# Kernel optimization log

Hardware: AMD Instinct MI355X
Metric: run time of the kernel (lower is better)

Reference implementation:

```python
import jax, jax.numpy as jnp
import numpy as np

LATENT = 1024
HIDDEN = 4096
ENC = 1024
HEADS = 16
HEAD_DIM = LATENT // HEADS
B, SQ, SK = 4, 1024, 1024
EPS = 1e-5


def _linear(x, w, b):
    # torch nn.Linear: y = x @ w.T + b, w shape (out, in)
    return jnp.einsum('bsi,oi->bso', x, w) + b


def _mha(Q, K, wq, bq, wk, bk, wv, bv, wo, bo):
    Bq, Sq, _ = Q.shape
    Sk = K.shape[1]
    Qp = _linear(Q, wq, bq).reshape(Bq, Sq, HEADS, HEAD_DIM)
    Kp = _linear(K, wk, bk).reshape(Bq, Sk, HEADS, HEAD_DIM)
    Vp = _linear(K, wv, bv).reshape(Bq, Sk, HEADS, HEAD_DIM)
    # NOTE: original scales by 1/sqrt(latent_size), not 1/sqrt(head_dim)
    E = jnp.einsum('bqhd,bkhd->bhqk', Qp, Kp) / np.sqrt(LATENT).astype(np.float32)
    A = jax.nn.softmax(E, axis=-1)
    O = jnp.einsum('bhqk,bkhd->bqhd', A, Vp).reshape(Bq, Sq, LATENT)
    return _linear(O, wo, bo)


def _ln(x, g, b):
    mu = jnp.mean(x, axis=-1, keepdims=True)
    var = jnp.mean((x - mu) ** 2, axis=-1, keepdims=True)
    return (x - mu) * jax.lax.rsqrt(var + EPS) * g + b


def setup_inputs() -> dict:
    key = jax.random.key(0)
    ks = jax.random.split(key, 32)
    s = 0.02
    d = {
        'Q': jax.random.normal(ks[0], (B, SQ, LATENT), jnp.float32),
        'K': jax.random.normal(ks[1], (B, SK, ENC), jnp.float32),
        'a1_wq': jax.random.normal(ks[2], (LATENT, LATENT)) * s,
        'a1_bq': jnp.zeros((LATENT,)),
        'a1_wk': jax.random.normal(ks[3], (LATENT, LATENT)) * s,
        'a1_bk': jnp.zeros((LATENT,)),
        'a1_wv': jax.random.normal(ks[4], (LATENT, LATENT)) * s,
        'a1_bv': jnp.zeros((LATENT,)),
        'a1_wo': jax.random.normal(ks[5], (LATENT, LATENT)) * s,
        'a1_bo': jnp.zeros((LATENT,)),
        'a2_wq': jax.random.normal(ks[6], (LATENT, LATENT)) * s,
        'a2_bq': jnp.zeros((LATENT,)),
        'a2_wk': jax.random.normal(ks[7], (LATENT, ENC)) * s,
        'a2_bk': jnp.zeros((LATENT,)),
        'a2_wv': jax.random.normal(ks[8], (LATENT, ENC)) * s,
        'a2_bv': jnp.zeros((LATENT,)),
        'a2_wo': jax.random.normal(ks[9], (LATENT, LATENT)) * s,
        'a2_bo': jnp.zeros((LATENT,)),
        'fc_w1': jax.random.normal(ks[10], (HIDDEN, LATENT)) * s,
        'fc_b1': jnp.zeros((HIDDEN,)),
        'fc_w2': jax.random.normal(ks[11], (LATENT, HIDDEN)) * s,
        'fc_b2': jnp.zeros((LATENT,)),
        'ln0_g': jnp.ones((LATENT,)), 'ln0_b': jnp.zeros((LATENT,)),
        'ln1_g': jnp.ones((LATENT,)), 'ln1_b': jnp.zeros((LATENT,)),
        'ln2_g': jnp.ones((LATENT,)), 'ln2_b': jnp.zeros((LATENT,)),
    }
    return d


def reference(Q, K, a1_wq, a1_bq, a1_wk, a1_bk, a1_wv, a1_bv, a1_wo, a1_bo,
              a2_wq, a2_bq, a2_wk, a2_bk, a2_wv, a2_bv, a2_wo, a2_bo,
              fc_w1, fc_b1, fc_w2, fc_b2,
              ln0_g, ln0_b, ln1_g, ln1_b, ln2_g, ln2_b):
    # self-attention block
    A1 = _mha(Q, Q, a1_wq, a1_bq, a1_wk, a1_bk, a1_wv, a1_bv, a1_wo, a1_bo)
    X = _ln(Q + A1, ln0_g, ln0_b)
    # cross-attention block
    A2 = _mha(X, K, a2_wq, a2_bq, a2_wk, a2_bk, a2_wv, a2_bv, a2_wo, a2_bo)
    X = _ln(X + A2, ln1_g, ln1_b)
    # FFN: Linear -> ReLU -> Linear
    FC = _linear(jax.nn.relu(_linear(X, fc_w1, fc_b1)), fc_w2, fc_b2)
    X = _ln(X + FC, ln2_g, ln2_b)
    return X
```

## Files before the change

### kernel.cpp

```cpp
#include <hip/hip_runtime.h>
#include <hip/hip_bf16.h>
#include <math.h>

#define LATENT 1024
#define HIDDEN 4096
#define HEADS 16
#define HEAD_DIM 64
#define BATCH 4
#define SQL 1024
#define SKL 1024

typedef __bf16 bf16;
typedef __attribute__((ext_vector_type(4))) __bf16 bf16x4;
typedef __attribute__((ext_vector_type(8))) __bf16 bf16x8;
typedef __attribute__((ext_vector_type(4))) float f32x4;

#define MFMA16 __builtin_amdgcn_mfma_f32_16x16x32_bf16

__device__ __forceinline__ void async_ld16(const bf16* g, bf16* l) {
    __builtin_amdgcn_global_load_lds(
        (const __attribute__((address_space(1))) unsigned int*)g,
        (__attribute__((address_space(3))) unsigned int*)l,
        16, 0, 0);
}

__global__ void detect_dtype(const void* g, int* flag) {
    if (threadIdx.x == 0) *flag = (*(const float*)g == 1.0f) ? 1 : 0;
}

struct CanonArgs {
    const void* src[28];
    bf16* dst[28];
    int n[28];
};

__global__ __launch_bounds__(256) void canonicalize(CanonArgs a, const int* flagp) {
    const int buf = blockIdx.y;
    const int n = a.n[buf];
    const int i0 = (blockIdx.x * 256 + threadIdx.x) * 8;
    if (i0 >= n) return;
    bf16* dst = a.dst[buf];
    if (*flagp) {
        const float* s = (const float*)a.src[buf];
        float4 u0 = *(const float4*)(s + i0);
        float4 u1 = *(const float4*)(s + i0 + 4);
        bf16x8 o;
        o[0] = (bf16)u0.x; o[1] = (bf16)u0.y; o[2] = (bf16)u0.z; o[3] = (bf16)u0.w;
        o[4] = (bf16)u1.x; o[5] = (bf16)u1.y; o[6] = (bf16)u1.z; o[7] = (bf16)u1.w;
        *(bf16x8*)(dst + i0) = o;
    } else {
        *(bf16x8*)(dst + i0) = *(const bf16x8*)((const bf16*)a.src[buf] + i0);
    }
}

template<bool RELU>
__global__ __launch_bounds__(256, 2)
void gemm8(const bf16* __restrict__ A, const bf16* __restrict__ W,
           const bf16* __restrict__ bias,
           bf16* __restrict__ out0, bf16* __restrict__ out1, bf16* __restrict__ outT,
           int M, int N, int K, int nNormal, int ostride) {
    constexpr int AE   = 128 * 32;
    constexpr int BE   = 256 * 32;
    constexpr int BUFE = AE + BE;
    __shared__ alignas(16) bf16 smem[3 * BUFE];
    const int tid  = threadIdx.x;
    const int w    = tid >> 6;
    const int lane = tid & 63;
    const int quad = lane >> 4;
    const int l16  = lane & 15;
    const int wrr  = w >> 1, wcc = w & 1;
    const int nx  = gridDim.x;
    const int nwg = nx * gridDim.y;
    int bid = blockIdx.y * nx + blockIdx.x;
    bid = (bid & 7) * (nwg >> 3) + (bid >> 3);
    const int bm = (bid / nx) * 128;
    const int bn = (bid % nx) * 256;

    f32x4 acc[4][8] = {};

    const bf16* gsrc[6]; int loff[6];
#pragma unroll
    for (int i = 0; i < 6; ++i) {
        const int s = tid + i * 256;
        if (s < 512) {
            const int r = s >> 2, cs = s & 3;
            gsrc[i] = A + (long)(bm + r) * K + ((cs ^ ((r >> 1) & 3)) << 3);
            loff[i] = s * 8;
        } else {
            const int sb = s - 512;
            const int r = sb >> 2, cs = sb & 3;
            gsrc[i] = W + (long)(bn + r) * K + ((cs ^ ((r >> 1) & 3)) << 3);
            loff[i] = AE + sb * 8;
        }
    }

    int offA[4], offB[8];
#pragma unroll
    for (int i = 0; i < 4; ++i) {
        const int r = wrr * 64 + i * 16 + l16;
        offA[i] = r * 32 + ((quad ^ ((r >> 1) & 3)) << 3);
    }
#pragma unroll
    for (int j = 0; j < 8; ++j) {
        const int r = wcc * 128 + j * 16 + l16;
        offB[j] = AE + r * 32 + ((quad ^ ((r >> 1) & 3)) << 3);
    }

#define STAGE_W(dst, tt)                                                       \
    {                                                                          \
        _Pragma("unroll")                                                      \
        for (int i_ = 0; i_ < 6; ++i_)                                         \
            async_ld16(gsrc[i_] + (tt) * 32, (dst) + loff[i_]);                \
    }

    const int NK = K >> 5;
    bf16 *p0 = smem, *p1 = smem + BUFE, *p2 = smem + 2 * BUFE;
    STAGE_W(p0, 0);
    STAGE_W(p1, 1);
    __asm__ volatile("s_waitcnt vmcnt(6)" ::: "memory");
    __builtin_amdgcn_s_barrier();
    __builtin_amdgcn_sched_barrier(0);

    for (int t = 0; t < NK; ++t) {
        if (t + 2 < NK) STAGE_W(p2, t + 2);
        bf16x8 af[4], bfv[8];
#pragma unroll
        for (int i = 0; i < 4; ++i) af[i]  = *(const bf16x8*)&p0[offA[i]];
#pragma unroll
        for (int j = 0; j < 8; ++j) bfv[j] = *(const bf16x8*)&p0[offB[j]];
#pragma unroll
        for (int j = 0; j < 8; ++j)
#pragma unroll
            for (int i = 0; i < 4; ++i)
                acc[i][j] = MFMA16(af[i], bfv[j], acc[i][j], 0, 0, 0);
        if (t + 2 < NK) {
            __asm__ volatile("s_waitcnt vmcnt(6)" ::: "memory");
        } else if (t + 1 < NK) {
            __asm__ volatile("s_waitcnt vmcnt(0)" ::: "memory");
        }
        if (t + 1 < NK) {
            __builtin_amdgcn_s_barrier();
            __builtin_amdgcn_sched_barrier(0);
        }
        bf16* tp = p0; p0 = p1; p1 = p2; p2 = tp;
    }
#undef STAGE_W

    float bvv[8];
#pragma unroll
    for (int j = 0; j < 8; ++j) bvv[j] = (float)bias[bn + wcc * 128 + j * 16 + l16];

    if (bn < nNormal) {
#pragma unroll
        for (int j = 0; j < 8; ++j) {
            const int colj = bn + wcc * 128 + j * 16;
            bf16* basej = out0;
            int cb = colj;
            if (out1 && cb >= 1024) { basej = out1; cb -= 1024; }
#pragma unroll
            for (int i = 0; i < 4; ++i) {
#pragma unroll
                for (int r = 0; r < 4; ++r) {
                    const int row = bm + wrr * 64 + i * 16 + quad * 4 + r;
                    float v = acc[i][j][r] + bvv[j];
                    if (RELU) v = fmaxf(v, 0.f);
                    basej[(long)row * ostride + cb + l16] = (bf16)v;
                }
            }
        }
    } else {
        const int n0v = bn - nNormal;
        __syncthreads();
#pragma unroll
        for (int p = 0; p < 4; ++p) {
            if (p) __syncthreads();
            if (wcc == (p >> 1)) {
#pragma unroll
                for (int i = 0; i < 4; ++i)
#pragma unroll
                    for (int jl = 0; jl < 4; ++jl) {
                        const int j = (p & 1) * 4 + jl;
                        const int colL = jl * 16 + l16;
                        const int rowL = wrr * 64 + i * 16 + quad * 4;
                        bf16x4 pk;
#pragma unroll
                        for (int r = 0; r < 4; ++r) pk[r] = (bf16)(acc[i][j][r] + bvv[j]);
                        *(bf16x4*)&smem[colL * 136 + rowL] = pk;
                    }
            }
            __syncthreads();
#pragma unroll
            for (int k = 0; k < 8; ++k) {
                const int c = tid + k * 256;
                const int rT = c >> 5, ch = c & 31;
                *(bf16x4*)&outT[(long)(n0v + p * 64 + rT) * M + bm + ch * 4] =
                    *(const bf16x4*)&smem[rT * 136 + ch * 4];
            }
        }
    }
}

template<int BN, bool RELU>
__global__ __launch_bounds__(256, 2)
void gemm2(const bf16* __restrict__ A, const bf16* __restrict__ W,
           const bf16* __restrict__ bias,
           bf16* __restrict__ out0, bf16* __restrict__ out1, bf16* __restrict__ outT,
           int M, int N, int K, int nNormal, int ostride) {
    constexpr int WAVES_N = BN / 64;
    constexpr int WAVES_M = 4 / WAVES_N;
    constexpr int WM = 128 / WAVES_M;
    constexpr int MI = WM / 16;
    constexpr int AE    = 128 * 64;
    constexpr int SLOTS = (128 + BN) * 8;
    constexpr int LPT   = SLOTS / 256;
    constexpr int BUFSZ = (128 + BN) * 64;
    __shared__ alignas(16) bf16 smem[2 * BUFSZ];
    const int tid  = threadIdx.x;
    const int w    = tid >> 6;
    const int lane = tid & 63;
    const int quad = lane >> 4;
    const int l16  = lane & 15;
    const int bm = blockIdx.y * 128;
    const int bn = blockIdx.x * BN;
    const int wr = w / WAVES_N, wc = w % WAVES_N;
    const int pp = l16 >> 1;

    f32x4 acc[MI][4] = {};

    const bf16* gsrc[LPT]; int loff[LPT];
#pragma unroll
    for (int i = 0; i < LPT; ++i) {
        const int s = tid + i * 256;
        if (s < 1024) {
            const int r = s >> 3, cs = s & 7;
            gsrc[i] = A + (long)(bm + r) * K + ((cs ^ ((r >> 1) & 7)) << 3);
            loff[i] = s * 8;
        } else {
            const int sb = s - 1024;
            const int r = sb >> 3, cs = sb & 7;
            gsrc[i] = W + (long)(bn + r) * K + ((cs ^ ((r >> 1) & 7)) << 3);
            loff[i] = AE + sb * 8;
        }
    }

    int offA[MI], offB[4];
#pragma unroll
    for (int i = 0; i < MI; ++i)
        offA[i] = (wr * WM + i * 16 + l16) * 64 + ((quad ^ pp) << 3);
#pragma unroll
    for (int j = 0; j < 4; ++j)
        offB[j] = AE + (wc * 64 + j * 16 + l16) * 64 + ((quad ^ pp) << 3);

#define STAGE_G(bufp, kk)                                                      \
    {                                                                          \
        bf16* bb_ = smem + (bufp) * BUFSZ;                                     \
        _Pragma("unroll")                                                      \
        for (int i_ = 0; i_ < LPT; ++i_)                                       \
            async_ld16(gsrc[i_] + (kk), bb_ + loff[i_]);                       \
    }

    STAGE_G(0, 0);
    __asm__ volatile("s_waitcnt vmcnt(0)" ::: "memory");
    __builtin_amdgcn_s_barrier();
    __builtin_amdgcn_sched_barrier(0);

    int cur = 0;
    for (int k0 = 0; k0 < K; k0 += 64) {
        if (k0 + 64 < K) STAGE_G(cur ^ 1, k0 + 64);
        const bf16* lbuf = smem + cur * BUFSZ;
#pragma unroll
        for (int ks = 0; ks < 2; ++ks) {
            bf16x8 af[MI], bfv[4];
#pragma unroll
            for (int i = 0; i < MI; ++i)
                af[i] = *(const bf16x8*)&lbuf[offA[i] ^ (ks << 5)];
#pragma unroll
            for (int j = 0; j < 4; ++j)
                bfv[j] = *(const bf16x8*)&lbuf[offB[j] ^ (ks << 5)];
#pragma unroll
            for (int i = 0; i < MI; ++i)
#pragma unroll
                for (int j = 0; j < 4; ++j)
                    acc[i][j] = MFMA16(af[i], bfv[j], acc[i][j], 0, 0, 0);
        }
        __asm__ volatile("s_waitcnt vmcnt(0)" ::: "memory");
        __builtin_amdgcn_s_barrier();
        __builtin_amdgcn_sched_barrier(0);
        cur ^= 1;
    }
#undef STAGE_G

    float bvv[4];
#pragma unroll
    for (int j = 0; j < 4; ++j) bvv[j] = (float)bias[bn + wc * 64 + j * 16 + l16];

    if (bn < nNormal) {
        bf16* base = out0;
        int colb = bn;
        if (out1 && colb >= 1024) { base = out1; colb -= 1024; }
#pragma unroll
        for (int i = 0; i < MI; ++i) {
#pragma unroll
            for (int r = 0; r < 4; ++r) {
                const int row = bm + wr * WM + i * 16 + quad * 4 + r;
#pragma unroll
                for (int j = 0; j < 4; ++j) {
                    float v = acc[i][j][r] + bvv[j];
                    if (RELU) v = fmaxf(v, 0.f);
                    base[(long)row * ostride + colb + wc * 64 + j * 16 + l16] = (bf16)v;
                }
            }
        }
    } else {
        const int n0v = bn - nNormal;
        __syncthreads();
#pragma unroll
        for (int p = 0; p < 2; ++p) {
            if (p) __syncthreads();
            if (wc == p) {
#pragma unroll
                for (int i = 0; i < MI; ++i)
#pragma unroll
                    for (int j = 0; j < 4; ++j) {
                        const int colL = j * 16 + l16;
                        const int rowL = wr * WM + i * 16 + quad * 4;
                        bf16x4 pk;
#pragma unroll
                        for (int r = 0; r < 4; ++r) pk[r] = (bf16)(acc[i][j][r] + bvv[j]);
                        *(bf16x4*)&smem[colL * 136 + rowL] = pk;
                    }
            }
            __syncthreads();
#pragma unroll
            for (int k = 0; k < 8; ++k) {
                const int c = tid + k * 256;
                const int rL = c >> 5, ch = c & 31;
                *(bf16x4*)&outT[(long)(n0v + p * 64 + rL) * M + bm + ch * 4] =
                    *(const bf16x4*)&smem[rL * 136 + ch * 4];
            }
        }
    }
}

__global__ __launch_bounds__(256, 3)
void attn2(const bf16* __restrict__ Qp, const bf16* __restrict__ Kp,
           const bf16* __restrict__ Vt, bf16* __restrict__ O) {
    __shared__ alignas(16) bf16 lQ[64 * 64];
    __shared__ alignas(16) bf16 lK[2][64 * 64];
    __shared__ alignas(16) bf16 lV[2][64 * 64];
    __shared__ alignas(16) bf16 lP[4][16 * 64];
    const int tid  = threadIdx.x;
    const int w    = tid >> 6;
    const int lane = tid & 63;
    const int quad = lane >> 4;
    const int l16  = lane & 15;
    const int pp   = l16 >> 1;
    const int b  = blockIdx.z;
    const int h  = blockIdx.y;
    const int q0 = blockIdx.x * 64;

#pragma unroll
    for (int s = 0; s < 2; ++s) {
        const int c = w * 128 + s * 64 + lane;
        const int row = c >> 3;
        const int ch = (((c & 7) ^ ((row >> 1) & 7)) << 3);
        async_ld16(Qp + (long)(b * SQL + q0 + row) * LATENT + h * 64 + ch, lQ + c * 8);
    }
#define STAGE_KV(buf, kt)                                                        \
    {                                                                            \
        _Pragma("unroll")                                                        \
        for (int s = 0; s < 2; ++s) {                                            \
            const int c = w * 128 + s * 64 + lane;                               \
            const int row = c >> 3;                                              \
            const int ch = (((c & 7) ^ ((row >> 1) & 7)) << 3);                  \
            async_ld16(Kp + (long)(b * SKL + (kt) * 64 + row) * LATENT + h * 64 + ch, \
                       &lK[buf][c * 8]);                                         \
            async_ld16(Vt + (long)(h * 64 + row) * (BATCH * SKL) + b * SKL + (kt) * 64 + ch, \
                       &lV[buf][c * 8]);                                         \
        }                                                                        \
    }
    STAGE_KV(0, 0);
    __syncthreads();

    const int aqoff = (w * 16 + l16) * 64 + ((quad ^ pp) << 3);
    bf16x8 aq[2];
    aq[0] = *(const bf16x8*)&lQ[aqoff];
    aq[1] = *(const bf16x8*)&lQ[aqoff ^ 32];
    int kvb[4];
#pragma unroll
    for (int j = 0; j < 4; ++j)
        kvb[j] = (j * 16 + l16) * 64 + ((quad ^ pp) << 3);
    const int apb = l16 * 64 + ((quad ^ pp) << 3);

    f32x4 o_acc[4] = {};
    float lsum[4] = {0.f, 0.f, 0.f, 0.f};

    for (int kt = 0; kt < SKL / 64; ++kt) {
        const int cur = kt & 1;
        if (kt < SKL / 64 - 1) STAGE_KV(cur ^ 1, kt + 1);

        f32x4 s4[4] = {};
        __builtin_amdgcn_s_setprio(1);
#pragma unroll
        for (int ks = 0; ks < 2; ++ks)
#pragma unroll
            for (int j = 0; j < 4; ++j) {
                bf16x8 bk = *(const bf16x8*)&lK[cur][kvb[j] ^ (ks << 5)];
                s4[j] = MFMA16(aq[ks], bk, s4[j], 0, 0, 0);
            }
        __builtin_amdgcn_s_setprio(0);

#pragma unroll
        for (int r = 0; r < 4; ++r) {
            const int psx = ((quad * 2 + (r >> 1)) & 7) << 3;
#pragma unroll
            for (int j = 0; j < 4; ++j) {
                const float p = __expf(s4[j][r] * 0.03125f);
                lsum[r] += p;
                lP[w][(quad * 4 + r) * 64 + ((j * 16 + l16) ^ psx)] = (bf16)p;
            }
        }
        __asm__ volatile("s_waitcnt lgkmcnt(0)" ::: "memory");

        __builtin_amdgcn_s_setprio(1);
#pragma unroll
        for (int ks = 0; ks < 2; ++ks) {
            bf16x8 ap = *(const bf16x8*)&lP[w][apb ^ (ks << 5)];
#pragma unroll
            for (int j = 0; j < 4; ++j) {
                bf16x8 bv = *(const bf16x8*)&lV[cur][kvb[j] ^ (ks << 5)];
                o_acc[j] = MFMA16(ap, bv, o_acc[j], 0, 0, 0);
            }
        }
        __builtin_amdgcn_s_setprio(0);
        __syncthreads();
    }

#pragma unroll
    for (int r = 0; r < 4; ++r) {
#pragma unroll
        for (int off = 1; off <= 8; off <<= 1)
            lsum[r] += __shfl_xor(lsum[r], off, 64);
    }
#pragma unroll
    for (int r = 0; r < 4; ++r) {
        const float inv = 1.f / lsum[r];
        const int row = q0 + w * 16 + quad * 4 + r;
#pragma unroll
        for (int j = 0; j < 4; ++j)
            O[(long)(b * SQL + row) * LATENT + h * 64 + j * 16 + l16] = (bf16)(o_acc[j][r] * inv);
    }
#undef STAGE_KV
}

template<bool F32OUT>
__global__ __launch_bounds__(256)
void ln_kernel(const bf16* __restrict__ res, const bf16* __restrict__ y,
               const bf16* __restrict__ g, const bf16* __restrict__ bta,
               bf16* __restrict__ outres, void* __restrict__ outb) {
    const int row = blockIdx.x;
    const int tid = threadIdx.x;
    const long base = (long)row * LATENT;
    const int c = tid * 4;
    bf16x4 rv = *(const bf16x4*)&res[base + c];
    bf16x4 yv = *(const bf16x4*)&y[base + c];
    float x[4];
    float s1 = 0.f, s2 = 0.f;
#pragma unroll
    for (int i = 0; i < 4; ++i) {
        float v = (float)rv[i] + (float)yv[i];
        x[i] = v; s1 += v; s2 += v * v;
    }
#pragma unroll
    for (int off = 32; off >= 1; off >>= 1) {
        s1 += __shfl_xor(s1, off, 64);
        s2 += __shfl_xor(s2, off, 64);
    }
    __shared__ float ps1[4], ps2[4];
    const int w = tid >> 6, lane = tid & 63;
    if (lane == 0) { ps1[w] = s1; ps2[w] = s2; }
    __syncthreads();
    s1 = ps1[0] + ps1[1] + ps1[2] + ps1[3];
    s2 = ps2[0] + ps2[1] + ps2[2] + ps2[3];
    const float mu = s1 * (1.f / LATENT);
    const float var = s2 * (1.f / LATENT) - mu * mu;
    const float rstd = rsqrtf(var + 1e-5f);
    bf16x4 gv = *(const bf16x4*)&g[c];
    bf16x4 bv = *(const bf16x4*)&bta[c];
    float o[4];
#pragma unroll
    for (int i = 0; i < 4; ++i)
        o[i] = (x[i] - mu) * rstd * (float)gv[i] + (float)bv[i];
    if (F32OUT) {
        float4 f; f.x = o[0]; f.y = o[1]; f.z = o[2]; f.w = o[3];
        *(float4*)&((float*)outb)[base + c] = f;
    } else {
        bf16x4 bo;
#pragma unroll
        for (int i = 0; i < 4; ++i) bo[i] = (bf16)o[i];
        *(bf16x4*)&((bf16*)outb)[base + c] = bo;
        if (outres) *(bf16x4*)&outres[base + c] = bo;
    }
}

extern "C" void kernel_launch(void* const* d_in, const int* in_sizes, int n_in,
                              void* d_out, int out_size, void* d_ws, size_t ws_size,
                              hipStream_t stream) {
    char* ws = (char*)d_ws;

    static const int order[28] = {2, 4, 6, 3, 5, 7, 12, 14, 13, 15,
                                  0, 1, 8, 9, 10, 11, 16, 17, 18, 19,
                                  20, 21, 22, 23, 24, 25, 26, 27};
    size_t coff[28];
    size_t cur = 256;
    for (int k = 0; k < 28; ++k) {
        const int i = order[k];
        coff[i] = cur;
        cur += (((size_t)in_sizes[i] * 2) + 255) & ~(size_t)255;
    }
    const size_t canon_end = (cur + 255) & ~(size_t)255;
    const size_t MB8 = 8ull << 20;
    const size_t need = canon_end + 7 * MB8;
    const bool full = ws_size >= need;

    const bf16* cv[28];
    if (full) {
        int* flag = (int*)ws;
        detect_dtype<<<dim3(1), dim3(64), 0, stream>>>(d_in[22], flag);
        CanonArgs ca;
        for (int i = 0; i < 28; ++i) {
            ca.src[i] = d_in[i];
            ca.dst[i] = (bf16*)(ws + coff[i]);
            ca.n[i]   = in_sizes[i];
            cv[i]     = (const bf16*)(ws + coff[i]);
        }
        canonicalize<<<dim3(2048, 28), dim3(256), 0, stream>>>(ca, flag);
    } else {
        for (int i = 0; i < 28; ++i) cv[i] = (const bf16*)d_in[i];
    }

    const size_t base = full ? canon_end : 0;
    bf16* Xres = (bf16*)(ws + base);
    bf16* Yf   = (bf16*)(ws + base + 1 * MB8);
    bf16* Xb   = (bf16*)(ws + base + 2 * MB8);
    bf16* Qp   = (bf16*)(ws + base + 3 * MB8);
    bf16* Kp   = (bf16*)(ws + base + 4 * MB8);
    bf16* Vt   = (bf16*)(ws + base + 5 * MB8);
    bf16* AttO = (bf16*)(ws + base + 6 * MB8);
    bf16* H    = Qp;

    const bf16 *Qc = cv[0], *Kc = cv[1];
    const int M = BATCH * SQL;
    dim3 blk(256);
    dim3 ga(SQL / 64, HEADS, BATCH);

    gemm8<false><<<dim3(3072 / 256, M / 128), blk, 0, stream>>>(
        Qc, cv[2], cv[3], Qp, Kp, Vt, M, 3072, LATENT, 2048, 1024);
    attn2<<<ga, blk, 0, stream>>>(Qp, Kp, Vt, AttO);
    gemm2<64, false><<<dim3(1024 / 64, M / 128), blk, 0, stream>>>(
        AttO, cv[8], cv[9], Yf, nullptr, nullptr, M, 1024, LATENT, 1024, 1024);
    ln_kernel<false><<<dim3(M), blk, 0, stream>>>(Qc, Yf, cv[22], cv[23], Xres, Xb);

    gemm2<64, false><<<dim3(1024 / 64, M / 128), blk, 0, stream>>>(
        Xb, cv[10], cv[11], Qp, nullptr, nullptr, M, 1024, LATENT, 1024, 1024);
    gemm8<false><<<dim3(2048 / 256, M / 128), blk, 0, stream>>>(
        Kc, cv[12], cv[13], Kp, nullptr, Vt, M, 2048, LATENT, 1024, 1024);
    attn2<<<ga, blk, 0, stream>>>(Qp, Kp, Vt, AttO);
    gemm2<64, false><<<dim3(1024 / 64, M / 128), blk, 0, stream>>>(
        AttO, cv[16], cv[17], Yf, nullptr, nullptr, M, 1024, LATENT, 1024, 1024);
    ln_kernel<false><<<dim3(M), blk, 0, stream>>>(Xres, Yf, cv[24], cv[25], Xres, Xb);

    gemm8<true><<<dim3(4096 / 256, M / 128), blk, 0, stream>>>(
        Xb, cv[18], cv[19], H, nullptr, nullptr, M, HIDDEN, LATENT, 4096, 4096);
    gemm2<64, false><<<dim3(1024 / 64, M / 128), blk, 0, stream>>>(
        H, cv[20], cv[21], Yf, nullptr, nullptr, M, 1024, HIDDEN, 1024, 1024);
    ln_kernel<true><<<dim3(M), blk, 0, stream>>>(Xres, Yf, cv[26], cv[27], nullptr, d_out);
}
```

Before: 480.7 us.

## Process 128 query rows per attention block to reuse K/V tiles

Each attention workgroup now handles 128 query rows instead of 64, with every wave computing two 16-row query tiles against the same K/V tiles held in LDS. This halves the global K/V traffic and the LDS K/V staging per query row, and gives each wave more independent MFMA work. In exchange it uses more registers and LDS (launch bounds drop to 2 blocks per CU), and the grid shrinks to 512 blocks, which lowers occupancy and parallelism.

Result: faster. 471.2 us (-2.0%).

```diff
diff --git a/kernel.cpp b/kernel.cpp
--- a/kernel.cpp
+++ b/kernel.cpp
@@ -342,13 +342,13 @@
     }
 }
 
-__global__ __launch_bounds__(256, 3)
+__global__ __launch_bounds__(256, 2)
 void attn2(const bf16* __restrict__ Qp, const bf16* __restrict__ Kp,
            const bf16* __restrict__ Vt, bf16* __restrict__ O) {
-    __shared__ alignas(16) bf16 lQ[64 * 64];
+    __shared__ alignas(16) bf16 lQ[128 * 64];
     __shared__ alignas(16) bf16 lK[2][64 * 64];
     __shared__ alignas(16) bf16 lV[2][64 * 64];
-    __shared__ alignas(16) bf16 lP[4][16 * 64];
+    __shared__ alignas(16) bf16 lP[4][32 * 64];
     const int tid  = threadIdx.x;
     const int w    = tid >> 6;
     const int lane = tid & 63;
@@ -357,11 +357,11 @@
     const int pp   = l16 >> 1;
     const int b  = blockIdx.z;
     const int h  = blockIdx.y;
-    const int q0 = blockIdx.x * 64;
-
-#pragma unroll
-    for (int s = 0; s < 2; ++s) {
-        const int c = w * 128 + s * 64 + lane;
+    const int q0 = blockIdx.x * 128;
+
+#pragma unroll
+    for (int s = 0; s < 4; ++s) {
+        const int c = s * 256 + tid;
         const int row = c >> 3;
         const int ch = (((c & 7) ^ ((row >> 1) & 7)) << 3);
         async_ld16(Qp + (long)(b * SQL + q0 + row) * LATENT + h * 64 + ch, lQ + c * 8);
@@ -382,42 +382,54 @@
     STAGE_KV(0, 0);
     __syncthreads();
 
-    const int aqoff = (w * 16 + l16) * 64 + ((quad ^ pp) << 3);
-    bf16x8 aq[2];
-    aq[0] = *(const bf16x8*)&lQ[aqoff];
-    aq[1] = *(const bf16x8*)&lQ[aqoff ^ 32];
+    bf16x8 aq0[2], aq1[2];
+    {
+        const int b0 = (w * 32 + l16) * 64 + ((quad ^ pp) << 3);
+        aq0[0] = *(const bf16x8*)&lQ[b0];
+        aq0[1] = *(const bf16x8*)&lQ[b0 ^ 32];
+        const int b1 = (w * 32 + 16 + l16) * 64 + ((quad ^ pp) << 3);
+        aq1[0] = *(const bf16x8*)&lQ[b1];
+        aq1[1] = *(const bf16x8*)&lQ[b1 ^ 32];
+    }
     int kvb[4];
 #pragma unroll
     for (int j = 0; j < 4; ++j)
         kvb[j] = (j * 16 + l16) * 64 + ((quad ^ pp) << 3);
     const int apb = l16 * 64 + ((quad ^ pp) << 3);
 
-    f32x4 o_acc[4] = {};
-    float lsum[4] = {0.f, 0.f, 0.f, 0.f};
+    f32x4 o_acc0[4] = {}, o_acc1[4] = {};
+    float lsum0[4] = {0.f, 0.f, 0.f, 0.f};
+    float lsum1[4] = {0.f, 0.f, 0.f, 0.f};
 
     for (int kt = 0; kt < SKL / 64; ++kt) {
         const int cur = kt & 1;
         if (kt < SKL / 64 - 1) STAGE_KV(cur ^ 1, kt + 1);
 
-        f32x4 s4[4] = {};
+        f32x4 s40[4] = {}, s41[4] = {};
         __builtin_amdgcn_s_setprio(1);
 #pragma unroll
         for (int ks = 0; ks < 2; ++ks)
 #pragma unroll
             for (int j = 0; j < 4; ++j) {
                 bf16x8 bk = *(const bf16x8*)&lK[cur][kvb[j] ^ (ks << 5)];
-                s4[j] = MFMA16(aq[ks], bk, s4[j], 0, 0, 0);
+                s40[j] = MFMA16(aq0[ks], bk, s40[j], 0, 0, 0);
+                s41[j] = MFMA16(aq1[ks], bk, s41[j], 0, 0, 0);
             }
         __builtin_amdgcn_s_setprio(0);
 
 #pragma unroll
         for (int r = 0; r < 4; ++r) {
             const int psx = ((quad * 2 + (r >> 1)) & 7) << 3;
+            const int ro = (quad * 4 + r) * 64;
 #pragma unroll
             for (int j = 0; j < 4; ++j) {
-                const float p = __expf(s4[j][r] * 0.03125f);
-                lsum[r] += p;
-                lP[w][(quad * 4 + r) * 64 + ((j * 16 + l16) ^ psx)] = (bf16)p;
+                const int cx = (j * 16 + l16) ^ psx;
+                const float p0 = __expf(s40[j][r] * 0.03125f);
+                lsum0[r] += p0;
+                lP[w][ro + cx] = (bf16)p0;
+                const float p1 = __expf(s41[j][r] * 0.03125f);
+                lsum1[r] += p1;
+                lP[w][1024 + ro + cx] = (bf16)p1;
             }
         }
         __asm__ volatile("s_waitcnt lgkmcnt(0)" ::: "memory");
@@ -425,11 +437,13 @@
         __builtin_amdgcn_s_setprio(1);
 #pragma unroll
         for (int ks = 0; ks < 2; ++ks) {
-            bf16x8 ap = *(const bf16x8*)&lP[w][apb ^ (ks << 5)];
+            bf16x8 ap0 = *(const bf16x8*)&lP[w][apb ^ (ks << 5)];
+            bf16x8 ap1 = *(const bf16x8*)&lP[w][1024 + (apb ^ (ks << 5))];
 #pragma unroll
             for (int j = 0; j < 4; ++j) {
                 bf16x8 bv = *(const bf16x8*)&lV[cur][kvb[j] ^ (ks << 5)];
-                o_acc[j] = MFMA16(ap, bv, o_acc[j], 0, 0, 0);
+                o_acc0[j] = MFMA16(ap0, bv, o_acc0[j], 0, 0, 0);
+                o_acc1[j] = MFMA16(ap1, bv, o_acc1[j], 0, 0, 0);
             }
         }
         __builtin_amdgcn_s_setprio(0);
@@ -439,16 +453,23 @@
 #pragma unroll
     for (int r = 0; r < 4; ++r) {
 #pragma unroll
-        for (int off = 1; off <= 8; off <<= 1)
-            lsum[r] += __shfl_xor(lsum[r], off, 64);
+        for (int off = 1; off <= 8; off <<= 1) {
+            lsum0[r] += __shfl_xor(lsum0[r], off, 64);
+            lsum1[r] += __shfl_xor(lsum1[r], off, 64);
+        }
     }
 #pragma unroll
     for (int r = 0; r < 4; ++r) {
-        const float inv = 1.f / lsum[r];
-        const int row = q0 + w * 16 + quad * 4 + r;
+        const int row0 = q0 + w * 32 + quad * 4 + r;
+        const float inv0 = 1.f / lsum0[r];
 #pragma unroll
         for (int j = 0; j < 4; ++j)
-            O[(long)(b * SQL + row) * LATENT + h * 64 + j * 16 + l16] = (bf16)(o_acc[j][r] * inv);
+            O[(long)(b * SQL + row0) * LATENT + h * 64 + j * 16 + l16] = (bf16)(o_acc0[j][r] * inv0);
+        const int row1 = row0 + 16;
+        const float inv1 = 1.f / lsum1[r];
+#pragma unroll
+        for (int j = 0; j < 4; ++j)
+            O[(long)(b * SQL + row1) * LATENT + h * 64 + j * 16 + l16] = (bf16)(o_acc1[j][r] * inv1);
     }
 #undef STAGE_KV
 }
@@ -552,7 +573,7 @@
     const bf16 *Qc = cv[0], *Kc = cv[1];
     const int M = BATCH * SQL;
     dim3 blk(256);
-    dim3 ga(SQL / 64, HEADS, BATCH);
+    dim3 ga(SQL / 128, HEADS, BATCH);
 
     gemm8<false><<<dim3(3072 / 256, M / 128), blk, 0, stream>>>(
         Qc, cv[2], cv[3], Qp, Kp, Vt, M, 3072, LATENT, 2048, 1024);
```
